# Kernel tuning notes

Hardware: AMD Instinct MI355X
Metric: run time of the kernel (lower is better)

Reference implementation:

```python
import jax, jax.numpy as jnp
import numpy as np

N, E, D_IN, H, M, C, B = 50000, 800000, 256, 128, 64, 4, 128
NH, HD = 8, H // 8


def setup_inputs() -> dict:
    key = jax.random.key(0)
    ks = jax.random.split(key, 24)
    s = 0.05
    rn = lambda k, shp: (jax.random.normal(k, shp) * s).astype(jnp.float32)
    return {
        "x": jax.random.normal(ks[0], (N, D_IN), dtype=jnp.float32),
        "edge_index": jax.random.randint(ks[1], (2, E), 0, N),
        "batch": jnp.sort(jax.random.randint(ks[2], (N,), 0, B)),
        # feature_transform: Linear(D_IN->H) + LayerNorm(H)
        "w1": rn(ks[3], (D_IN, H)), "b1": jnp.zeros((H,), jnp.float32),
        "ln_g": jnp.ones((H,), jnp.float32), "ln_b": jnp.zeros((H,), jnp.float32),
        # 3 GCNConv(H->H) layers
        "gw1": rn(ks[4], (H, H)), "gb1": jnp.zeros((H,), jnp.float32),
        "gw2": rn(ks[5], (H, H)), "gb2": jnp.zeros((H,), jnp.float32),
        "gw3": rn(ks[6], (H, H)), "gb3": jnp.zeros((H,), jnp.float32),
        # memory bank + MultiheadAttention(H, 8 heads), torch layout (out,in)
        "memory_bank": jax.random.normal(ks[7], (M, H), dtype=jnp.float32),
        "in_proj_w": rn(ks[8], (3 * H, H)), "in_proj_b": jnp.zeros((3 * H,), jnp.float32),
        "out_w": rn(ks[9], (H, H)), "out_b": jnp.zeros((H,), jnp.float32),
        # classifier: Linear(2H->H) -> ReLU -> Linear(H->C)
        "cw1": rn(ks[10], (2 * H, H)), "cb1": jnp.zeros((H,), jnp.float32),
        "cw2": rn(ks[11], (H, C)), "cb2": jnp.zeros((C,), jnp.float32),
    }


def _layer_norm(x, g, b, eps=1e-5):
    mu = jnp.mean(x, axis=-1, keepdims=True)
    var = jnp.var(x, axis=-1, keepdims=True)
    return (x - mu) * jax.lax.rsqrt(var + eps) * g + b


def _gcn(x, W, b, row, col, norm):
    # PyG GCNConv: x' = D^-1/2 (A+I) D^-1/2 (x W) + b, aggregated at col (target)
    xw = x @ W
    msg = xw[row] * norm[:, None]                      # [E+N, H]
    out = jax.ops.segment_sum(msg, col, num_segments=N)
    return out + b


def reference(x, edge_index, batch, w1, b1, ln_g, ln_b, gw1, gb1, gw2, gb2, gw3, gb3,
              memory_bank, in_proj_w, in_proj_b, out_w, out_b, cw1, cb1, cw2, cb2):
    # feature transform (dropout is identity in eval)
    h = _layer_norm(jax.nn.relu(x @ w1 + b1), ln_g, ln_b)

    # GCN normalization with self-loops
    sl = jnp.arange(N)
    row = jnp.concatenate([edge_index[0], sl])
    col = jnp.concatenate([edge_index[1], sl])
    deg = jax.ops.segment_sum(jnp.ones_like(col, dtype=h.dtype), col, num_segments=N)
    dis = jax.lax.rsqrt(deg)                           # deg >= 1 from self-loops
    norm = dis[row] * dis[col]

    for W, b in ((gw1, gb1), (gw2, gb2), (gw3, gb3)):
        h = jax.nn.relu(_gcn(h, W, b, row, col, norm))

    # global mean pool per graph
    sums = jax.ops.segment_sum(h, batch, num_segments=B)
    cnts = jax.ops.segment_sum(jnp.ones((N,), h.dtype), batch, num_segments=B)
    pooled = sums / jnp.maximum(cnts, 1.0)[:, None]    # [B, H]

    # memory attention: query = pooled (len 1), kv = memory bank (shared)
    q = pooled @ in_proj_w[:H].T + in_proj_b[:H]       # [B, H]
    k = memory_bank @ in_proj_w[H:2 * H].T + in_proj_b[H:2 * H]  # [M, H]
    v = memory_bank @ in_proj_w[2 * H:].T + in_proj_b[2 * H:]    # [M, H]
    qh = q.reshape(B, NH, HD)
    kh = k.reshape(M, NH, HD)
    vh = v.reshape(M, NH, HD)
    scores = jnp.einsum('bhd,mhd->bhm', qh, kh) / jnp.sqrt(jnp.float32(HD))
    p = jax.nn.softmax(scores, axis=-1)
    attn = jnp.einsum('bhm,mhd->bhd', p, vh).reshape(B, H)
    mem = attn @ out_w.T + out_b                       # [B, H]

    # classifier on [pooled, memory_enhanced]
    z = jnp.concatenate([pooled, mem], axis=-1)        # [B, 2H]
    z = jax.nn.relu(z @ cw1 + cb1)
    return z @ cw2 + cb2                               # [B, C]
```

## Files before the change

kernel.cpp:

```cpp
#include <hip/hip_runtime.h>

#define NN 50000
#define EE 800000
#define DIN 256
#define H 128
#define MM 64
#define CC 4
#define BB 128
#define NHEAD 8
#define HDIM 16

#define NRW 50
#define RNODES 1000
#define NSB 625
#define ESL 1280

typedef _Float16 f16x8 __attribute__((ext_vector_type(8)));
typedef _Float16 f16x4 __attribute__((ext_vector_type(4)));
typedef float f32x4 __attribute__((ext_vector_type(4)));


__launch_bounds__(256)
__global__ void ecount(const int* __restrict__ col, int* __restrict__ bcnt) {
    __shared__ int hist[NRW];
    int b = blockIdx.x, t = threadIdx.x;
    if (t < NRW) hist[t] = 0;
    __syncthreads();
    int e0 = b * ESL;
    #pragma unroll
    for (int i = 0; i < ESL / 256; i++) {
        int c = col[e0 + t + i * 256];
        atomicAdd(&hist[c / RNODES], 1);
    }
    __syncthreads();
    if (t < NRW) bcnt[t * NSB + b] = hist[t];
}

__global__ void escan(const int* __restrict__ bcnt, int* __restrict__ sbase,
                      int* __restrict__ rbase) {
    __shared__ int rt[NRW];
    int t = threadIdx.x;
    if (t < NRW) {
        int s = 0;
        for (int b = 0; b < NSB; b++) s += bcnt[t * NSB + b];
        rt[t] = s;
    }
    __syncthreads();
    if (t == 0) {
        int run = 0;
        for (int r = 0; r < NRW; r++) { rbase[r] = run; run += rt[r]; }
    }
    __syncthreads();
    if (t < NRW) {
        int run = rbase[t];
        for (int b = 0; b < NSB; b++) { sbase[t * NSB + b] = run; run += bcnt[t * NSB + b]; }
    }
}

__launch_bounds__(256)
__global__ void escatter(const int* __restrict__ row, const int* __restrict__ col,
                         const int* __restrict__ sbase, int2* __restrict__ ebuf) {
    __shared__ int cur[NRW];
    int b = blockIdx.x, t = threadIdx.x;
    if (t < NRW) cur[t] = sbase[t * NSB + b];
    __syncthreads();
    int e0 = b * ESL;
    #pragma unroll
    for (int i = 0; i < ESL / 256; i++) {
        int e = e0 + t + i * 256;
        int c = col[e];
        int u = row[e];
        int r = c / RNODES;
        int p = atomicAdd(&cur[r], 1);
        ebuf[p] = make_int2(u, c - r * RNODES);
    }
}

__launch_bounds__(512)
__global__ void csr_build(const int2* __restrict__ ebuf, const int* __restrict__ rbase,
                          int* __restrict__ degcnt, int* __restrict__ offs,
                          float* __restrict__ dis, int* __restrict__ csr) {
    __shared__ int hist[RNODES];
    __shared__ int cur[RNODES];
    __shared__ int sb[512];
    int r = blockIdx.x, t = threadIdx.x;
    int r0 = r * RNODES;
    int rb = rbase[r];
    int re = (r + 1 < NRW) ? rbase[r + 1] : EE;
    for (int i = t; i < RNODES; i += 512) hist[i] = 0;
    __syncthreads();
    for (int e = rb + t; e < re; e += 512) atomicAdd(&hist[ebuf[e].y], 1);
    __syncthreads();
    int i0 = 2 * t, i1 = 2 * t + 1;
    int d0 = (i0 < RNODES) ? hist[i0] : 0;
    int d1 = (i1 < RNODES) ? hist[i1] : 0;
    int ps = d0 + d1;
    sb[t] = ps;
    __syncthreads();
    for (int off = 1; off < 512; off <<= 1) {
        int x = (t >= off) ? sb[t - off] : 0;
        __syncthreads();
        sb[t] += x;
        __syncthreads();
    }
    int excl = sb[t] - ps;
    if (i0 < RNODES) {
        cur[i0] = excl;
        degcnt[r0 + i0] = d0;
        offs[r0 + i0] = rb + excl;
        dis[r0 + i0] = rsqrtf((float)(d0 + 1));
    }
    if (i1 < RNODES) {
        cur[i1] = excl + d0;
        degcnt[r0 + i1] = d1;
        offs[r0 + i1] = rb + excl + d0;
        dis[r0 + i1] = rsqrtf((float)(d1 + 1));
    }
    __syncthreads();
    for (int e = rb + t; e < re; e += 512) {
        int2 ed = ebuf[e];
        int p = atomicAdd(&cur[ed.y], 1);
        csr[rb + p] = ed.x;
    }
}


__global__ void graph_bounds(const int* __restrict__ batch, int* __restrict__ gstart) {
    int v = blockIdx.x * blockDim.x + threadIdx.x;
    if (v >= NN) return;
    int b = batch[v];
    if (v == 0) {
        for (int g = 0; g <= b; g++) gstart[g] = 0;
    } else {
        int pb = batch[v - 1];
        for (int g = pb + 1; g <= b; g++) gstart[g] = v;
    }
    if (v == NN - 1) {
        for (int g = b + 1; g <= BB; g++) gstart[g] = NN;
    }
}


__global__ void wsplit_all(const float* __restrict__ w1, const float* __restrict__ gw1,
                           const float* __restrict__ gw2, const float* __restrict__ gw3,
                           _Float16* __restrict__ wf1, _Float16* __restrict__ wfg1,
                           _Float16* __restrict__ wfg2, _Float16* __restrict__ wfg3) {
    int b = blockIdx.x;
    int l = threadIdx.x;
    const float* Wg; _Float16* outw; int KT, f;
    if (b < 64)       { Wg = w1;  outw = wf1;  KT = 8; f = b; }
    else if (b < 96)  { Wg = gw1; outw = wfg1; KT = 4; f = b - 64; }
    else if (b < 128) { Wg = gw2; outw = wfg2; KT = 4; f = b - 96; }
    else              { Wg = gw3; outw = wfg3; KT = 4; f = b - 128; }
    int kt = f >> 3, ct = f & 7;
    int k0 = kt * 32 + (l >> 4) * 8;
    int c = ct * 16 + (l & 15);
    f16x8 hi, lo;
    #pragma unroll
    for (int j = 0; j < 8; j++) {
        float w = Wg[(size_t)(k0 + j) * H + c];
        _Float16 hh = (_Float16)w;
        hi[j] = hh;
        lo[j] = (_Float16)(w - (float)hh);
    }
    *reinterpret_cast<f16x8*>(outw + ((size_t)f * 64 + l) * 8) = hi;
    *reinterpret_cast<f16x8*>(outw + ((size_t)KT * 8 * 64 * 8) + ((size_t)f * 64 + l) * 8) = lo;
}


template <int K, bool LN, int OMODE, bool POOL, int AIN>
__launch_bounds__(256)
__global__ void mfma_linear(const void* __restrict__ Ap, const _Float16* __restrict__ Wf,
                            const float* __restrict__ bias,
                            const float* __restrict__ ln_g, const float* __restrict__ ln_b,
                            const float* __restrict__ dis, const int* __restrict__ batch,
                            void* __restrict__ outp) {
    constexpr int KT = K / 32;
    __shared__ __align__(16) _Float16 stage[2][8192];
    int t = threadIdx.x;
    int wv = t >> 6, l = t & 63;
    int lm = l & 15, lg = l >> 4;
    int rowBase = blockIdx.x * 64;
    int arow = rowBase + wv * 16 + lm;
    int arc = min(arow, NN - 1);
    const float* A32 = (const float*)Ap;
    const _Float16* A16 = (const _Float16*)Ap;
    const f16x8* __restrict__ BhG = reinterpret_cast<const f16x8*>(Wf);
    const f16x8* __restrict__ BlG = BhG + KT * 8 * 64;

    auto stage_kt = [&](int b, int kt) {
        f16x8* dstH = reinterpret_cast<f16x8*>(&stage[b][0]);
        f16x8* dstL = reinterpret_cast<f16x8*>(&stage[b][4096]);
        int wo = wv * 128 + l;
        #pragma unroll
        for (int i = 0; i < 2; i++) {
            int o = wo + i * 64;
            dstH[o] = BhG[(size_t)kt * 512 + o];
            dstL[o] = BlG[(size_t)kt * 512 + o];
        }
    };

    f32x4 acc[8];
    #pragma unroll
    for (int ct = 0; ct < 8; ct++) acc[ct] = (f32x4){0.f, 0.f, 0.f, 0.f};

    stage_kt(0, 0);
    float4 a0c = {}, a1c = {}; f16x8 a16c = {};
    if constexpr (AIN == 0) {
        const float* ap = A32 + (size_t)arc * K + lg * 8;
        a0c = *(const float4*)ap; a1c = *(const float4*)(ap + 4);
    } else {
        a16c = *(const f16x8*)(A16 + (size_t)arc * K + lg * 8);
    }
    __syncthreads();
    int buf = 0;
    for (int kt = 0; kt < KT; kt++) {
        float4 a0n = {}, a1n = {}; f16x8 a16n = {};
        if (kt + 1 < KT) {
            stage_kt(buf ^ 1, kt + 1);
            if constexpr (AIN == 0) {
                const float* ap = A32 + (size_t)arc * K + (kt + 1) * 32 + lg * 8;
                a0n = *(const float4*)ap; a1n = *(const float4*)(ap + 4);
            } else {
                a16n = *(const f16x8*)(A16 + (size_t)arc * K + (kt + 1) * 32 + lg * 8);
            }
        }
        f16x8 ah, al;
        if constexpr (AIN == 0) {
            float av[8] = {a0c.x, a0c.y, a0c.z, a0c.w, a1c.x, a1c.y, a1c.z, a1c.w};
            #pragma unroll
            for (int j = 0; j < 8; j++) {
                _Float16 hh = (_Float16)av[j];
                ah[j] = hh;
                al[j] = (_Float16)(av[j] - (float)hh);
            }
        } else {
            ah = a16c;
        }
        #pragma unroll
        for (int ct = 0; ct < 8; ct++) {
            f16x8 bh = *reinterpret_cast<const f16x8*>(&stage[buf][(ct * 64 + l) * 8]);
            f16x8 bl = *reinterpret_cast<const f16x8*>(&stage[buf][4096 + (ct * 64 + l) * 8]);
            acc[ct] = __builtin_amdgcn_mfma_f32_16x16x32_f16(ah, bh, acc[ct], 0, 0, 0);
            acc[ct] = __builtin_amdgcn_mfma_f32_16x16x32_f16(ah, bl, acc[ct], 0, 0, 0);
            if constexpr (AIN == 0)
                acc[ct] = __builtin_amdgcn_mfma_f32_16x16x32_f16(al, bh, acc[ct], 0, 0, 0);
        }
        __syncthreads();
        buf ^= 1;
        a0c = a0n; a1c = a1n; a16c = a16n;
    }

    float bv[8], gv[8], lbv[8];
    #pragma unroll
    for (int ct = 0; ct < 8; ct++) {
        int c = ct * 16 + lm;
        bv[ct] = bias[c];
        if constexpr (LN) { gv[ct] = ln_g[c]; lbv[ct] = ln_b[c]; }
    }

    float vals[4][8];
    #pragma unroll
    for (int q = 0; q < 4; q++) {
        float s = 0.f, sq = 0.f;
        #pragma unroll
        for (int ct = 0; ct < 8; ct++) {
            float v = fmaxf(acc[ct][q] + bv[ct], 0.f);
            vals[q][ct] = v;
            s += v; sq += v * v;
        }
        if constexpr (LN) {
            #pragma unroll
            for (int m = 1; m < 16; m <<= 1) {
                s  += __shfl_xor(s,  m, 64);
                sq += __shfl_xor(sq, m, 64);
            }
            float mean = s * (1.f / 128.f);
            float var  = sq * (1.f / 128.f) - mean * mean;
            float inv  = rsqrtf(var + 1e-5f);
            #pragma unroll
            for (int ct = 0; ct < 8; ct++)
                vals[q][ct] = (vals[q][ct] - mean) * inv * gv[ct] + lbv[ct];
        }
    }

    if constexpr (POOL) {
        __shared__ float tile[64][129];
        __shared__ int bl64[64];
        float* psums = (float*)outp;
        #pragma unroll
        for (int q = 0; q < 4; q++) {
            int r64 = wv * 16 + lg * 4 + q;
            #pragma unroll
            for (int ct = 0; ct < 8; ct++)
                tile[r64][ct * 16 + lm] = vals[q][ct];
        }
        if (t < 64) bl64[t] = batch[min(rowBase + t, NN - 1)];
        __syncthreads();
        if (t < H) {
            float pacc = 0.f;
            int curb = bl64[0];
            int rmax = min(64, NN - rowBase);
            for (int r = 0; r < rmax; r++) {
                int b = bl64[r];
                if (b != curb) {
                    atomicAdd(&psums[curb * H + t], pacc);
                    pacc = 0.f; curb = b;
                }
                pacc += tile[r][t];
            }
            atomicAdd(&psums[curb * H + t], pacc);
        }
    } else {
        #pragma unroll
        for (int q = 0; q < 4; q++) {
            int rr = rowBase + wv * 16 + lg * 4 + q;
            if (rr < NN) {
                if constexpr (OMODE == 1) {
                    _Float16* o16 = (_Float16*)outp;
                    float sc = dis[rr];
                    #pragma unroll
                    for (int ct = 0; ct < 8; ct++)
                        o16[(size_t)rr * H + ct * 16 + lm] = (_Float16)(vals[q][ct] * sc);
                } else {
                    float* o32 = (float*)outp;
                    #pragma unroll
                    for (int ct = 0; ct < 8; ct++)
                        o32[(size_t)rr * H + ct * 16 + lm] = vals[q][ct];
                }
            }
        }
    }
}


__launch_bounds__(256)
__global__ void agg_kernel(const _Float16* __restrict__ g16, const int* __restrict__ offs,
                           const int* __restrict__ degcnt, const int* __restrict__ csr,
                           const float* __restrict__ dis, _Float16* __restrict__ out16) {
    __shared__ int idx[8][64];
    int grp = threadIdx.x >> 5;
    int l = threadIdx.x & 31;
    int v = blockIdx.x * 8 + grp;
    int beg = offs[v], cnt = degcnt[v];
    idx[grp][l]      = (l      < cnt) ? csr[beg + l]      : v;
    idx[grp][l + 32] = (l + 32 < cnt) ? csr[beg + l + 32] : v;

    const f16x4* __restrict__ G = reinterpret_cast<const f16x4*>(g16);
    float dv = dis[v];
    f16x4 gvh = G[(size_t)v * 32 + l];
    float4 gv = make_float4((float)gvh[0], (float)gvh[1], (float)gvh[2], (float)gvh[3]);
    float4 acc = gv;
    int n0 = min(cnt, 64);
    int m0 = (n0 + 7) & ~7;

    for (int i = 0; i < m0; i += 8) {
        f16x4 tv[8];
        #pragma unroll
        for (int jj = 0; jj < 8; jj++)
            tv[jj] = G[(size_t)idx[grp][i + jj] * 32 + l];
        #pragma unroll
        for (int jj = 0; jj < 8; jj++) {
            acc.x += (float)tv[jj][0];
            acc.y += (float)tv[jj][1];
            acc.z += (float)tv[jj][2];
            acc.w += (float)tv[jj][3];
        }
    }
    float pad = (float)(m0 - n0);
    acc.x -= pad * gv.x; acc.y -= pad * gv.y;
    acc.z -= pad * gv.z; acc.w -= pad * gv.w;

    for (int i = 64; i < cnt; i++) {
        f16x4 a = G[(size_t)csr[beg + i] * 32 + l];
        acc.x += (float)a[0]; acc.y += (float)a[1];
        acc.z += (float)a[2]; acc.w += (float)a[3];
    }
    f16x4 o;
    o[0] = (_Float16)(dv * acc.x); o[1] = (_Float16)(dv * acc.y);
    o[2] = (_Float16)(dv * acc.z); o[3] = (_Float16)(dv * acc.w);
    reinterpret_cast<f16x4*>(out16)[(size_t)v * 32 + l] = o;
}


__global__ void kv_kernel(const float* __restrict__ mb, const float* __restrict__ ipw,
                          const float* __restrict__ ipb,
                          float* __restrict__ kbuf, float* __restrict__ vbuf) {
    __shared__ float rowv[H];
    int m = blockIdx.x, i = threadIdx.x;
    rowv[i] = mb[m * H + i];
    __syncthreads();
    float ak = 0.f, av = 0.f;
    for (int j = 0; j < H; j++) {
        float x = rowv[j];
        ak = fmaf(x, ipw[(size_t)(H + i) * H + j], ak);
        av = fmaf(x, ipw[(size_t)(2 * H + i) * H + j], av);
    }
    kbuf[m * H + i] = ak + ipb[H + i];
    vbuf[m * H + i] = av + ipb[2 * H + i];
}


__launch_bounds__(128)
__global__ void attn_kernel(const float* __restrict__ psums, const int* __restrict__ gstart,
                            const float* __restrict__ kbuf, const float* __restrict__ vbuf,
                            const float* __restrict__ ipw, const float* __restrict__ ipb,
                            const float* __restrict__ out_w, const float* __restrict__ out_b,
                            const float* __restrict__ cw1, const float* __restrict__ cb1,
                            const float* __restrict__ cw2, const float* __restrict__ cb2,
                            float* __restrict__ out) {
    __shared__ float pooled[H], q[H], attn[H], z[2 * H], c1[H], sc[NHEAD * MM];
    int b = blockIdx.x, t = threadIdx.x;
    float cn = (float)max(gstart[b + 1] - gstart[b], 1);
    float pv = psums[b * H + t] / cn;
    pooled[t] = pv;
    z[t] = pv;
    __syncthreads();
    float a = 0.f;
    for (int j = 0; j < H; j++) a = fmaf(pooled[j], ipw[(size_t)t * H + j], a);
    q[t] = a + ipb[t];
    __syncthreads();
    for (int sidx = t; sidx < NHEAD * MM; sidx += 128) {
        int hh = sidx >> 6, m = sidx & 63;
        float s2 = 0.f;
        for (int d = 0; d < HDIM; d++)
            s2 = fmaf(q[hh * HDIM + d], kbuf[m * H + hh * HDIM + d], s2);
        sc[sidx] = s2 * 0.25f;
    }
    __syncthreads();
    if (t < NHEAD) {
        float mx = -1e30f;
        for (int m = 0; m < MM; m++) mx = fmaxf(mx, sc[t * MM + m]);
        float ssum = 0.f;
        for (int m = 0; m < MM; m++) { float e = expf(sc[t * MM + m] - mx); sc[t * MM + m] = e; ssum += e; }
        float inv = 1.f / ssum;
        for (int m = 0; m < MM; m++) sc[t * MM + m] *= inv;
    }
    __syncthreads();
    {
        int hh = t >> 4;
        float a2 = 0.f;
        for (int m = 0; m < MM; m++) a2 = fmaf(sc[hh * MM + m], vbuf[m * H + t], a2);
        attn[t] = a2;
    }
    __syncthreads();
    float mm = 0.f;
    for (int j = 0; j < H; j++) mm = fmaf(attn[j], out_w[(size_t)t * H + j], mm);
    z[H + t] = mm + out_b[t];
    __syncthreads();
    float cc = 0.f;
    for (int j = 0; j < 2 * H; j++) cc = fmaf(z[j], cw1[(size_t)j * H + t], cc);
    c1[t] = fmaxf(cc + cb1[t], 0.f);
    __syncthreads();
    if (t < CC) {
        float o = 0.f;
        for (int j = 0; j < H; j++) o = fmaf(c1[j], cw2[j * CC + t], o);
        out[b * CC + t] = o + cb2[t];
    }
}


extern "C" void kernel_launch(void* const* d_in, const int* in_sizes, int n_in,
                              void* d_out, int out_size, void* d_ws, size_t ws_size,
                              hipStream_t stream) {
    const float* x      = (const float*)d_in[0];
    const int*   eidx   = (const int*)d_in[1];
    const int*   batch  = (const int*)d_in[2];
    const float* w1     = (const float*)d_in[3];
    const float* b1     = (const float*)d_in[4];
    const float* ln_g   = (const float*)d_in[5];
    const float* ln_b   = (const float*)d_in[6];
    const float* gw1    = (const float*)d_in[7];
    const float* gb1    = (const float*)d_in[8];
    const float* gw2    = (const float*)d_in[9];
    const float* gb2    = (const float*)d_in[10];
    const float* gw3    = (const float*)d_in[11];
    const float* gb3    = (const float*)d_in[12];
    const float* memb   = (const float*)d_in[13];
    const float* ipw    = (const float*)d_in[14];
    const float* ipb    = (const float*)d_in[15];
    const float* out_w  = (const float*)d_in[16];
    const float* out_b  = (const float*)d_in[17];
    const float* cw1    = (const float*)d_in[18];
    const float* cb1    = (const float*)d_in[19];
    const float* cw2    = (const float*)d_in[20];
    const float* cb2    = (const float*)d_in[21];

    const int* row = eidx;
    const int* col = eidx + EE;

    char* ws = (char*)d_ws;
    size_t off = 0;
    auto alloc = [&](size_t bytes) -> void* {
        void* p = ws + off;
        off += (bytes + 255) & ~(size_t)255;
        return p;
    };
    _Float16* a16 = (_Float16*)alloc((size_t)NN * H * 2);
    _Float16* g16 = (_Float16*)alloc((size_t)NN * H * 2);
    char*  zbeg   = ws + off;
    float* psums  = (float*)alloc((size_t)BB * H * 4);
    size_t zbytes = (size_t)((ws + off) - zbeg);
    int*   degcnt = (int*)alloc((size_t)NN * 4);
    float* dis    = (float*)alloc((size_t)NN * 4);
    int*   offs   = (int*)alloc((size_t)NN * 4);
    int*   csr    = (int*)alloc((size_t)EE * 4);
    int2*  ebuf   = (int2*)alloc((size_t)EE * 8);
    int*   bcnt   = (int*)alloc((size_t)NRW * NSB * 4);
    int*   sbase  = (int*)alloc((size_t)NRW * NSB * 4);
    int*   rbase  = (int*)alloc(256);
    int*   gstart = (int*)alloc((size_t)(BB + 1) * 4);
    float* kbuf   = (float*)alloc((size_t)MM * H * 4);
    float* vbuf   = (float*)alloc((size_t)MM * H * 4);
    _Float16* wf1 = (_Float16*)alloc((size_t)2 * DIN * H * 2);
    _Float16* wfg1 = (_Float16*)alloc((size_t)2 * H * H * 2);
    _Float16* wfg2 = (_Float16*)alloc((size_t)2 * H * H * 2);
    _Float16* wfg3 = (_Float16*)alloc((size_t)2 * H * H * 2);
    (void)ws_size; (void)in_sizes; (void)n_in; (void)out_size;

    hipMemsetAsync(zbeg, 0, zbytes, stream);

    ecount<<<NSB, 256, 0, stream>>>(col, bcnt);
    escan<<<1, 64, 0, stream>>>(bcnt, sbase, rbase);
    escatter<<<NSB, 256, 0, stream>>>(row, col, sbase, ebuf);
    csr_build<<<NRW, 512, 0, stream>>>(ebuf, rbase, degcnt, offs, dis, csr);

    graph_bounds<<<(NN + 255) / 256, 256, 0, stream>>>(batch, gstart);

    wsplit_all<<<160, 64, 0, stream>>>(w1, gw1, gw2, gw3, wf1, wfg1, wfg2, wfg3);

    const int LGRID = (NN + 63) / 64;
    const int AGRID = NN / 8;

    mfma_linear<DIN, true, 1, false, 0><<<LGRID, 256, 0, stream>>>(x, wf1, b1, ln_g, ln_b, dis, nullptr, g16);

    agg_kernel<<<AGRID, 256, 0, stream>>>(g16, offs, degcnt, csr, dis, a16);
    mfma_linear<H, false, 1, false, 1><<<LGRID, 256, 0, stream>>>(a16, wfg1, gb1, nullptr, nullptr, dis, nullptr, g16);
    agg_kernel<<<AGRID, 256, 0, stream>>>(g16, offs, degcnt, csr, dis, a16);
    mfma_linear<H, false, 1, false, 1><<<LGRID, 256, 0, stream>>>(a16, wfg2, gb2, nullptr, nullptr, dis, nullptr, g16);
    agg_kernel<<<AGRID, 256, 0, stream>>>(g16, offs, degcnt, csr, dis, a16);
    mfma_linear<H, false, 0, true, 1><<<LGRID, 256, 0, stream>>>(a16, wfg3, gb3, nullptr, nullptr, dis, batch, psums);

    kv_kernel<<<MM, H, 0, stream>>>(memb, ipw, ipb, kbuf, vbuf);
    attn_kernel<<<BB, H, 0, stream>>>(psums, gstart, kbuf, vbuf, ipw, ipb, out_w, out_b,
                                      cw1, cb1, cw2, cb2, (float*)d_out);
}
```

Measured before the change: 254.4 us.

## Parallelize bucket-offset scan across blocks and preload A rows in MFMA linear

Replaces the single-block serial escan, where 50 threads each walked 625 counts twice, with three kernels: a per-range parallel reduction, a tiny scan over range totals, and a per-range block-parallel prefix scan of the per-block counts. Separately, the MFMA linear kernel now loads the whole A row fragment for every k-tile into registers up front instead of prefetching one tile ahead, and fully unrolls the k-loop. This shortens the latency-bound serial scan and puts more global loads in flight, at the cost of two extra launches and higher register pressure (up to 16 float4 per thread), which may lower occupancy.

```diff
diff --git a/kernel.cpp b/kernel.cpp
--- a/kernel.cpp
+++ b/kernel.cpp
@@ -36,24 +36,49 @@
     if (t < NRW) bcnt[t * NSB + b] = hist[t];
 }
 
-__global__ void escan(const int* __restrict__ bcnt, int* __restrict__ sbase,
-                      int* __restrict__ rbase) {
-    __shared__ int rt[NRW];
-    int t = threadIdx.x;
-    if (t < NRW) {
-        int s = 0;
-        for (int b = 0; b < NSB; b++) s += bcnt[t * NSB + b];
-        rt[t] = s;
-    }
-    __syncthreads();
-    if (t == 0) {
+__launch_bounds__(256)
+__global__ void erange_tot(const int* __restrict__ bcnt, int* __restrict__ rtot) {
+    __shared__ int red[4];
+    int r = blockIdx.x, t = threadIdx.x;
+    int s = 0;
+    for (int b = t; b < NSB; b += 256) s += bcnt[r * NSB + b];
+    #pragma unroll
+    for (int m = 1; m < 64; m <<= 1) s += __shfl_xor(s, m, 64);
+    if ((t & 63) == 0) red[t >> 6] = s;
+    __syncthreads();
+    if (t == 0) rtot[r] = red[0] + red[1] + red[2] + red[3];
+}
+
+__global__ void rscan(const int* __restrict__ rtot, int* __restrict__ rbase) {
+    if (threadIdx.x == 0 && blockIdx.x == 0) {
         int run = 0;
-        for (int r = 0; r < NRW; r++) { rbase[r] = run; run += rt[r]; }
-    }
-    __syncthreads();
-    if (t < NRW) {
-        int run = rbase[t];
-        for (int b = 0; b < NSB; b++) { sbase[t * NSB + b] = run; run += bcnt[t * NSB + b]; }
+        for (int i = 0; i < NRW; i++) { rbase[i] = run; run += rtot[i]; }
+    }
+}
+
+__launch_bounds__(256)
+__global__ void esbase(const int* __restrict__ bcnt, const int* __restrict__ rbase,
+                       int* __restrict__ sbase) {
+    __shared__ int sb[256];
+    __shared__ int carry;
+    int r = blockIdx.x, t = threadIdx.x;
+    if (t == 0) carry = rbase[r];
+    __syncthreads();
+    for (int base = 0; base < NSB; base += 256) {
+        int b = base + t;
+        int v = (b < NSB) ? bcnt[r * NSB + b] : 0;
+        sb[t] = v;
+        __syncthreads();
+        for (int off = 1; off < 256; off <<= 1) {
+            int x = (t >= off) ? sb[t - off] : 0;
+            __syncthreads();
+            sb[t] += x;
+            __syncthreads();
+        }
+        if (b < NSB) sbase[r * NSB + b] = carry + sb[t] - v;
+        __syncthreads();
+        if (t == 255) carry += sb[255];
+        __syncthreads();
     }
 }
 
@@ -200,33 +225,33 @@
         }
     };
 
+    float4 aAll[16]; f16x8 aAll16[8];
+    if constexpr (AIN == 0) {
+        #pragma unroll
+        for (int kt = 0; kt < KT; kt++) {
+            const float* ap = A32 + (size_t)arc * K + kt * 32 + lg * 8;
+            aAll[2 * kt]     = *(const float4*)ap;
+            aAll[2 * kt + 1] = *(const float4*)(ap + 4);
+        }
+    } else {
+        #pragma unroll
+        for (int kt = 0; kt < KT; kt++)
+            aAll16[kt] = *(const f16x8*)(A16 + (size_t)arc * K + kt * 32 + lg * 8);
+    }
+
     f32x4 acc[8];
     #pragma unroll
     for (int ct = 0; ct < 8; ct++) acc[ct] = (f32x4){0.f, 0.f, 0.f, 0.f};
 
     stage_kt(0, 0);
-    float4 a0c = {}, a1c = {}; f16x8 a16c = {};
-    if constexpr (AIN == 0) {
-        const float* ap = A32 + (size_t)arc * K + lg * 8;
-        a0c = *(const float4*)ap; a1c = *(const float4*)(ap + 4);
-    } else {
-        a16c = *(const f16x8*)(A16 + (size_t)arc * K + lg * 8);
-    }
     __syncthreads();
     int buf = 0;
+    #pragma unroll
     for (int kt = 0; kt < KT; kt++) {
-        float4 a0n = {}, a1n = {}; f16x8 a16n = {};
-        if (kt + 1 < KT) {
-            stage_kt(buf ^ 1, kt + 1);
-            if constexpr (AIN == 0) {
-                const float* ap = A32 + (size_t)arc * K + (kt + 1) * 32 + lg * 8;
-                a0n = *(const float4*)ap; a1n = *(const float4*)(ap + 4);
-            } else {
-                a16n = *(const f16x8*)(A16 + (size_t)arc * K + (kt + 1) * 32 + lg * 8);
-            }
-        }
+        if (kt + 1 < KT) stage_kt(buf ^ 1, kt + 1);
         f16x8 ah, al;
         if constexpr (AIN == 0) {
+            float4 a0c = aAll[2 * kt], a1c = aAll[2 * kt + 1];
             float av[8] = {a0c.x, a0c.y, a0c.z, a0c.w, a1c.x, a1c.y, a1c.z, a1c.w};
             #pragma unroll
             for (int j = 0; j < 8; j++) {
@@ -235,7 +260,7 @@
                 al[j] = (_Float16)(av[j] - (float)hh);
             }
         } else {
-            ah = a16c;
+            ah = aAll16[kt];
         }
         #pragma unroll
         for (int ct = 0; ct < 8; ct++) {
@@ -248,7 +273,6 @@
         }
         __syncthreads();
         buf ^= 1;
-        a0c = a0n; a1c = a1n; a16c = a16n;
     }
 
     float bv[8], gv[8], lbv[8];
@@ -508,6 +532,7 @@
     int2*  ebuf   = (int2*)alloc((size_t)EE * 8);
     int*   bcnt   = (int*)alloc((size_t)NRW * NSB * 4);
     int*   sbase  = (int*)alloc((size_t)NRW * NSB * 4);
+    int*   rtot   = (int*)alloc(256);
     int*   rbase  = (int*)alloc(256);
     int*   gstart = (int*)alloc((size_t)(BB + 1) * 4);
     float* kbuf   = (float*)alloc((size_t)MM * H * 4);
@@ -521,7 +546,9 @@
     hipMemsetAsync(zbeg, 0, zbytes, stream);
 
     ecount<<<NSB, 256, 0, stream>>>(col, bcnt);
-    escan<<<1, 64, 0, stream>>>(bcnt, sbase, rbase);
+    erange_tot<<<NRW, 256, 0, stream>>>(bcnt, rtot);
+    rscan<<<1, 64, 0, stream>>>(rtot, rbase);
+    esbase<<<NRW, 256, 0, stream>>>(bcnt, rbase, sbase);
     escatter<<<NSB, 256, 0, stream>>>(row, col, sbase, ebuf);
     csr_build<<<NRW, 512, 0, stream>>>(ebuf, rbase, degcnt, offs, dis, csr);
 
```

Result: faster. 235.9 us (-7.3%).
